# Performance work log

Hardware: AMD Instinct MI355X
Metric: run time of the kernel (lower is better)

## Reference

```python
import jax, jax.numpy as jnp
import numpy as np

CHANNELS_CHOICE = np.array([8, 16, 24, 32, 40, 48, 56, 64])
MAX_C = 64
B, H, W_SP = 128, 32, 32
N_EDGES = 6
# edge list per intermediate node: (edge_weight_index, source_node_index)
EDGES = [[(0, 0)], [(1, 0), (2, 1)], [(3, 0), (4, 1), (5, 2)]]


def setup_inputs() -> dict:
    key = jax.random.key(0)
    k1, k2, k3, k4 = jax.random.split(key, 4)
    inputs = jax.random.normal(k1, (B, MAX_C, H, W_SP), dtype=jnp.float32)
    alphas1 = jax.random.uniform(k2, (8,), dtype=jnp.float32)  # input-width arch weights
    alphas2 = jax.random.uniform(k3, (8,), dtype=jnp.float32)  # output-width arch weights
    # shared master 3x3 conv weight per edge (OIHW)
    W = jax.random.normal(k4, (N_EDGES, MAX_C, MAX_C, 3, 3), dtype=jnp.float32) * 0.05
    return {"inputs": inputs, "alphas1": alphas1, "alphas2": alphas2, "W": W}


def _channel_scale(alphas1, alphas2, dtype):
    # mask[c, i] = 1 if channel c is inside width choice CHANNELS_CHOICE[i]
    mask = (jnp.arange(MAX_C)[:, None] < jnp.asarray(CHANNELS_CHOICE)[None, :]).astype(dtype)  # [64, 8]
    a_in = mask @ alphas1   # [64] cumulative input-channel weight
    a_out = mask @ alphas2  # [64] cumulative output-channel weight
    return a_out[:, None] * a_in[None, :]  # [64, 64]


def _edge(x, w, scale):
    # weighted-combi of all (c1, c2) channel-sliced sub-convs == one conv with scaled weight
    w_eff = w * scale[:, :, None, None]
    return jax.lax.conv_general_dilated(
        jax.nn.relu(x), w_eff, window_strides=(1, 1), padding="SAME",
        dimension_numbers=("NCHW", "OIHW", "NCHW"))


def reference(inputs, alphas1, alphas2, W):
    scale = _channel_scale(alphas1, alphas2, inputs.dtype)
    nodes = [inputs]
    for node_edges in EDGES:
        feat = 0.0
        for l, src in node_edges:
            feat = feat + _edge(nodes[src], W[l], scale)
        nodes.append(feat)
    return nodes[-1]
```

## Files before the change

kernel.cpp:

```cpp
#include <hip/hip_runtime.h>
#include <hip/hip_bf16.h>


typedef __bf16 bf16x8 __attribute__((ext_vector_type(8)));
typedef float floatx4 __attribute__((ext_vector_type(4)));
typedef unsigned int uint32;

#define PADW 34
#define PIMG (PADW * PADW)
#define ROWB (PADW * 64 * 2)
#define A_LDS (18 * ROWB)
#define A_CHUNKS (A_LDS / 16)
#define A_TAIL (A_CHUNKS - 9 * 512)
#define TAPB (64 * 64 * 2)
#define B_LDS (9 * TAPB)
#define SMEM_BYTES (A_LDS + B_LDS)

__device__ __forceinline__ void gld16(const char* g, char* l) {
    __builtin_amdgcn_global_load_lds(
        (const __attribute__((address_space(1))) uint32*)g,
        (__attribute__((address_space(3))) uint32*)l, 16, 0, 0);
}

__global__ __launch_bounds__(256) void pre_kernel(
    const float* __restrict__ in, const float* __restrict__ a1,
    const float* __restrict__ a2, const float* __restrict__ W,
    __hip_bfloat16* __restrict__ wt, __hip_bfloat16* __restrict__ r0,
    __hip_bfloat16* __restrict__ r1, __hip_bfloat16* __restrict__ r2) {
    __shared__ float tile[32][65];
    int blk = blockIdx.x;
    int tid = threadIdx.x;

    if (blk < 864) {
        int idx = blk * 256 + tid;
        int i = idx & 63;
        int o = (idx >> 6) & 63;
        int rest = idx >> 12;
        int t = rest % 9;
        int l = rest / 9;
        int ji = i >> 3, jo = o >> 3;
        float ain = 0.f, aout = 0.f;
#pragma unroll
        for (int j = 0; j < 8; ++j) {
            ain  += (j >= ji) ? a1[j] : 0.f;
            aout += (j >= jo) ? a2[j] : 0.f;
        }
        float v = W[(size_t)((l * 64 + o) * 64 + i) * 9 + t] * ain * aout;
        int os = ((o & 3) << 4) + (o >> 2);
        size_t e = (size_t)(l * 9 + t) * 4096 + os * 64 +
                   ((((i >> 3) ^ (os & 7)) << 3) + (i & 7));
        wt[e] = __float2bfloat16(v);
    } else if (blk < 992) {
        int b = blk - 864;
        __hip_bfloat16* bufs[3] = {r0, r1, r2};
#pragma unroll
        for (int f = 0; f < 3; ++f) {
            uint32* buf = (uint32*)(bufs[f] + (size_t)b * PIMG * 64);
            for (int idx = tid; idx < 132 * 32; idx += 256) {
                int slot = idx >> 5, u = idx & 31;
                int yy, xx;
                if (slot < 34)      { yy = 0;  xx = slot; }
                else if (slot < 68) { yy = 33; xx = slot - 34; }
                else { int s2 = slot - 68; yy = 1 + (s2 >> 1); xx = (s2 & 1) * 33; }
                buf[(size_t)(yy * PADW + xx) * 32 + u] = 0u;
            }
        }
    } else {
        int rb = blk - 992;
        int b = rb >> 5, y = rb & 31;
        int x = tid & 31, c0 = tid >> 5;
        const float* ip = in + ((size_t)b * 64 * 32 + y) * 32 + x;
#pragma unroll
        for (int cc = 0; cc < 8; ++cc) {
            int c = cc * 8 + c0;
            tile[x][c] = fmaxf(ip[(size_t)c * 1024], 0.f);
        }
        __syncthreads();
        int j = tid & 7, xq = tid >> 3;
        int p = (b * PADW + y + 1) * PADW + 1 + xq;
        alignas(16) __hip_bfloat16 hv[8];
#pragma unroll
        for (int k = 0; k < 8; ++k)
            hv[k] = __float2bfloat16(tile[xq][j * 8 + k]);
        *(uint4*)((char*)r0 + (size_t)p * 128 + ((j ^ (p & 7)) << 4)) =
            *(const uint4*)hv;
    }
}

template <int NSRC, bool FINAL>
__global__ __launch_bounds__(512, 1) void conv_stage(
    const __hip_bfloat16* __restrict__ s0,
    const __hip_bfloat16* __restrict__ s1,
    const __hip_bfloat16* __restrict__ s2,
    const __hip_bfloat16* __restrict__ wt,
    void* __restrict__ dstv, int l0) {
    extern __shared__ char smem[];
    char* smemB = smem + A_LDS;
    int tid = threadIdx.x;
    int wv = tid >> 6, lane = tid & 63;
    int quad = lane >> 4, l15 = lane & 15;
    int blk = blockIdx.x;
    int b = blk >> 1, y0 = (blk & 1) << 4;

    const char* srcs[3] = {(const char*)s0, (const char*)s1, (const char*)s2};
    const char* gW = (const char*)wt + (size_t)l0 * 9 * (size_t)TAPB;
    const size_t aOff = (size_t)(b * PADW + y0) * PADW * 128;

    auto stage_A = [&](int s) {
        const char* gA = srcs[s] + aOff;
#pragma unroll
        for (int it = 0; it < 10; ++it) {
            int c = it * 512 + tid;
            if (it < 9 || tid < A_TAIL)
                gld16(gA + (size_t)c * 16, smem + (it * 512 + wv * 64) * 16);
        }
    };
    auto stage_B = [&](int s) {
        const char* gB = gW + (size_t)s * 9 * TAPB;
#pragma unroll
        for (int it = 0; it < 9; ++it) {
            int c = it * 512 + tid;
            gld16(gB + (size_t)c * 16, smemB + (it * 512 + wv * 64) * 16);
        }
    };

    floatx4 acc[4][4];
#pragma unroll
    for (int m = 0; m < 4; ++m)
#pragma unroll
        for (int n = 0; n < 4; ++n) acc[m][n] = (floatx4){0.f, 0.f, 0.f, 0.f};

    stage_A(0);
    stage_B(0);
    __syncthreads();

    uint4 pfA[10];

#pragma unroll 1
    for (int s = 0; s < NSRC; ++s) {
        if (s + 1 < NSRC) {
            const char* gA = srcs[s + 1] + aOff;
#pragma unroll
            for (int it = 0; it < 10; ++it)
                pfA[it] = *(const uint4*)(gA + (size_t)(it * 512 + tid) * 16);
            __builtin_amdgcn_sched_barrier(0);
        }
#pragma unroll
        for (int tl = 0; tl < 9; ++tl) {
            const int ky = tl / 3, kx = tl % 3;
#pragma unroll
            for (int q = 0; q < 2; ++q) {
                bf16x8 Af[4], Bf[4];
#pragma unroll
                for (int m = 0; m < 4; ++m) {
                    int arow = 2 * wv + (m >> 1) + ky;
                    int apx  = ((m & 1) << 4) + l15 + kx;
                    int R = b * PADW + y0 + arow;
                    int slot = ((q << 2) + quad) ^ ((2 * R + apx) & 7);
                    Af[m] = *(const bf16x8*)(smem + arow * ROWB +
                                             apx * 128 + slot * 16);
                }
#pragma unroll
                for (int n = 0; n < 4; ++n) {
                    int o = (n << 4) + l15;
                    int slot = ((q << 2) + quad) ^ (l15 & 7);
                    Bf[n] = *(const bf16x8*)(smemB + tl * TAPB +
                                             o * 128 + slot * 16);
                }
                __builtin_amdgcn_s_setprio(1);
#pragma unroll
                for (int m = 0; m < 4; ++m)
#pragma unroll
                    for (int n = 0; n < 4; ++n)
                        acc[m][n] = __builtin_amdgcn_mfma_f32_16x16x32_bf16(
                            Af[m], Bf[n], acc[m][n], 0, 0, 0);
                __builtin_amdgcn_s_setprio(0);
            }
        }
        if (s + 1 < NSRC) {
            __syncthreads();
#pragma unroll
            for (int it = 0; it < 10; ++it)
                if (it < 9 || tid < A_TAIL)
                    *(uint4*)(smem + (size_t)(it * 512 + tid) * 16) = pfA[it];
            stage_B(s + 1);
            __syncthreads();
        }
    }

    if (FINAL) {
        float* out = (float*)dstv;
#pragma unroll
        for (int m = 0; m < 4; ++m) {
            int row = y0 + 2 * wv + (m >> 1);
#pragma unroll
            for (int n = 0; n < 4; ++n) {
                int o = (l15 << 2) + n;
                *(floatx4*)(out + (((size_t)b * 64 + o) * 32 + row) * 32 +
                            ((m & 1) << 4) + (quad << 2)) = acc[m][n];
            }
        }
    } else {
        __hip_bfloat16* out = (__hip_bfloat16*)dstv;
#pragma unroll
        for (int m = 0; m < 4; ++m) {
            int row = y0 + 2 * wv + (m >> 1);
#pragma unroll
            for (int r = 0; r < 4; ++r) {
                int x = ((m & 1) << 4) + (quad << 2) + r;
                int p = (b * PADW + row + 1) * PADW + x + 1;
                alignas(8) __hip_bfloat16 hv[4];
#pragma unroll
                for (int n = 0; n < 4; ++n)
                    hv[n] = __float2bfloat16(fmaxf(acc[m][n][r], 0.f));
                char* d8 = (char*)out + (size_t)p * 128 +
                           ((((l15 >> 1) ^ (p & 7)) << 4) + ((l15 & 1) << 3));
                *(uint2*)d8 = *(const uint2*)hv;
            }
        }
    }
}

extern "C" void kernel_launch(void* const* d_in, const int* in_sizes, int n_in,
                              void* d_out, int out_size, void* d_ws,
                              size_t ws_size, hipStream_t stream) {
    const float* inputs  = (const float*)d_in[0];
    const float* alphas1 = (const float*)d_in[1];
    const float* alphas2 = (const float*)d_in[2];
    const float* W       = (const float*)d_in[3];
    char* ws = (char*)d_ws;

    __hip_bfloat16* wt = (__hip_bfloat16*)(ws);
    __hip_bfloat16* r0 = (__hip_bfloat16*)(ws + ((size_t)1 << 20));
    __hip_bfloat16* r1 = (__hip_bfloat16*)(ws + ((size_t)20 << 20));
    __hip_bfloat16* r2 = (__hip_bfloat16*)(ws + ((size_t)40 << 20));
    float* out = (float*)d_out;

    (void)hipFuncSetAttribute((const void*)conv_stage<1, false>,
                              hipFuncAttributeMaxDynamicSharedMemorySize,
                              SMEM_BYTES);
    (void)hipFuncSetAttribute((const void*)conv_stage<2, false>,
                              hipFuncAttributeMaxDynamicSharedMemorySize,
                              SMEM_BYTES);
    (void)hipFuncSetAttribute((const void*)conv_stage<3, true>,
                              hipFuncAttributeMaxDynamicSharedMemorySize,
                              SMEM_BYTES);

    pre_kernel<<<864 + 128 + 4096, 256, 0, stream>>>(inputs, alphas1, alphas2,
                                                     W, wt, r0, r1, r2);
    conv_stage<1, false><<<256, 512, SMEM_BYTES, stream>>>(r0, r1, r2, wt,
                                                           (void*)r1, 0);
    conv_stage<2, false><<<256, 512, SMEM_BYTES, stream>>>(r0, r1, r2, wt,
                                                           (void*)r2, 1);
    conv_stage<3, true ><<<256, 512, SMEM_BYTES, stream>>>(r0, r1, r2, wt,
                                                           (void*)out, 3);
}
```

Measured before the change: 169.9 us.

## Double-buffer LDS fragment loads and drop register prefetch of next source tile

The inner MFMA loop is flattened into 18 steps, and the A/B fragments for the next step are loaded from LDS into a second register buffer while the current step's MFMAs run. The register prefetch of the next source's A tile (ten uint4 per thread, global to registers to LDS) is removed. The next source is now loaded with direct global-to-LDS loads after the barrier. This hides LDS latency inside the MFMA loop and frees registers, but the global load of the next source is no longer overlapped with compute.

```diff
diff --git a/kernel.cpp b/kernel.cpp
--- a/kernel.cpp
+++ b/kernel.cpp
@@ -124,6 +124,28 @@
         }
     };
 
+    auto ldA = [&](int tl, int q, bf16x8 (&dst)[4]) {
+        const int ky = tl / 3, kx = tl % 3;
+#pragma unroll
+        for (int m = 0; m < 4; ++m) {
+            int arow = 2 * wv + (m >> 1) + ky;
+            int apx  = ((m & 1) << 4) + l15 + kx;
+            int R = b * PADW + y0 + arow;
+            int slot = ((q << 2) + quad) ^ ((2 * R + apx) & 7);
+            dst[m] = *(const bf16x8*)(smem + arow * ROWB + apx * 128 +
+                                      slot * 16);
+        }
+    };
+    auto ldB = [&](int tl, int q, bf16x8 (&dst)[4]) {
+#pragma unroll
+        for (int n = 0; n < 4; ++n) {
+            int o = (n << 4) + l15;
+            int slot = ((q << 2) + quad) ^ (l15 & 7);
+            dst[n] = *(const bf16x8*)(smemB + tl * TAPB + o * 128 +
+                                      slot * 16);
+        }
+    };
+
     floatx4 acc[4][4];
 #pragma unroll
     for (int m = 0; m < 4; ++m)
@@ -134,55 +156,31 @@
     stage_B(0);
     __syncthreads();
 
-    uint4 pfA[10];
-
 #pragma unroll 1
     for (int s = 0; s < NSRC; ++s) {
-        if (s + 1 < NSRC) {
-            const char* gA = srcs[s + 1] + aOff;
-#pragma unroll
-            for (int it = 0; it < 10; ++it)
-                pfA[it] = *(const uint4*)(gA + (size_t)(it * 512 + tid) * 16);
-            __builtin_amdgcn_sched_barrier(0);
-        }
-#pragma unroll
-        for (int tl = 0; tl < 9; ++tl) {
-            const int ky = tl / 3, kx = tl % 3;
-#pragma unroll
-            for (int q = 0; q < 2; ++q) {
-                bf16x8 Af[4], Bf[4];
-#pragma unroll
-                for (int m = 0; m < 4; ++m) {
-                    int arow = 2 * wv + (m >> 1) + ky;
-                    int apx  = ((m & 1) << 4) + l15 + kx;
-                    int R = b * PADW + y0 + arow;
-                    int slot = ((q << 2) + quad) ^ ((2 * R + apx) & 7);
-                    Af[m] = *(const bf16x8*)(smem + arow * ROWB +
-                                             apx * 128 + slot * 16);
-                }
-#pragma unroll
-                for (int n = 0; n < 4; ++n) {
-                    int o = (n << 4) + l15;
-                    int slot = ((q << 2) + quad) ^ (l15 & 7);
-                    Bf[n] = *(const bf16x8*)(smemB + tl * TAPB +
-                                             o * 128 + slot * 16);
-                }
-                __builtin_amdgcn_s_setprio(1);
-#pragma unroll
-                for (int m = 0; m < 4; ++m)
-#pragma unroll
-                    for (int n = 0; n < 4; ++n)
-                        acc[m][n] = __builtin_amdgcn_mfma_f32_16x16x32_bf16(
-                            Af[m], Bf[n], acc[m][n], 0, 0, 0);
-                __builtin_amdgcn_s_setprio(0);
-            }
+        bf16x8 fA[2][4], fB[2][4];
+        ldA(0, 0, fA[0]);
+        ldB(0, 0, fB[0]);
+#pragma unroll
+        for (int st = 0; st < 18; ++st) {
+            const int pb = st & 1;
+            if (st < 17) {
+                const int nt = (st + 1) >> 1, nq = (st + 1) & 1;
+                ldA(nt, nq, fA[pb ^ 1]);
+                ldB(nt, nq, fB[pb ^ 1]);
+            }
+            __builtin_amdgcn_s_setprio(1);
+#pragma unroll
+            for (int m = 0; m < 4; ++m)
+#pragma unroll
+                for (int n = 0; n < 4; ++n)
+                    acc[m][n] = __builtin_amdgcn_mfma_f32_16x16x32_bf16(
+                        fA[pb][m], fB[pb][n], acc[m][n], 0, 0, 0);
+            __builtin_amdgcn_s_setprio(0);
         }
         if (s + 1 < NSRC) {
             __syncthreads();
-#pragma unroll
-            for (int it = 0; it < 10; ++it)
-                if (it < 9 || tid < A_TAIL)
-                    *(uint4*)(smem + (size_t)(it * 512 + tid) * 16) = pfA[it];
+            stage_A(s + 1);
             stage_B(s + 1);
             __syncthreads();
         }
```

Result: faster. 148.9 us (-12.3%).

## Stream conv weights directly from global into registers, drop LDS B staging

Applied to the files above, without the earlier changes.

Re-lays out the preprocessed weight tensor in MFMA-fragment order so each lane can load its B operand fragments straight from global memory into registers, double-buffered per tap. The weight LDS region and its staging are removed, which shrinks shared memory to the activation tile only. The register prefetch of the next source's activations is also removed; the next source is now loaded into LDS synchronously after a barrier. This trades LDS traffic and capacity for more global/L2 reads per wave, higher register pressure, and an exposed activation load between sources.

```diff
diff --git a/kernel.cpp b/kernel.cpp
--- a/kernel.cpp
+++ b/kernel.cpp
@@ -5,6 +5,7 @@
 typedef __bf16 bf16x8 __attribute__((ext_vector_type(8)));
 typedef float floatx4 __attribute__((ext_vector_type(4)));
 typedef unsigned int uint32;
+typedef uint32 u32x4 __attribute__((ext_vector_type(4)));
 
 #define PADW 34
 #define PIMG (PADW * PADW)
@@ -13,8 +14,7 @@
 #define A_CHUNKS (A_LDS / 16)
 #define A_TAIL (A_CHUNKS - 9 * 512)
 #define TAPB (64 * 64 * 2)
-#define B_LDS (9 * TAPB)
-#define SMEM_BYTES (A_LDS + B_LDS)
+#define SMEM_BYTES A_LDS
 
 __device__ __forceinline__ void gld16(const char* g, char* l) {
     __builtin_amdgcn_global_load_lds(
@@ -47,9 +47,12 @@
         }
         float v = W[(size_t)((l * 64 + o) * 64 + i) * 9 + t] * ain * aout;
         int os = ((o & 3) << 4) + (o >> 2);
-        size_t e = (size_t)(l * 9 + t) * 4096 + os * 64 +
-                   ((((i >> 3) ^ (os & 7)) << 3) + (i & 7));
-        wt[e] = __float2bfloat16(v);
+        int n  = os >> 4, c15 = os & 15;
+        int q  = i >> 5, quad = (i >> 3) & 3, e = i & 7;
+        int ln = (quad << 4) + c15;
+        size_t idx2 = (size_t)(l * 9 + t) * 4096 + (((q << 2) + n) << 9) +
+                      (ln << 3) + e;
+        wt[idx2] = __float2bfloat16(v);
     } else if (blk < 992) {
         int b = blk - 864;
         __hip_bfloat16* bufs[3] = {r0, r1, r2};
@@ -95,7 +98,6 @@
     const __hip_bfloat16* __restrict__ wt,
     void* __restrict__ dstv, int l0) {
     extern __shared__ char smem[];
-    char* smemB = smem + A_LDS;
     int tid = threadIdx.x;
     int wv = tid >> 6, lane = tid & 63;
     int quad = lane >> 4, l15 = lane & 15;
@@ -115,14 +117,6 @@
                 gld16(gA + (size_t)c * 16, smem + (it * 512 + wv * 64) * 16);
         }
     };
-    auto stage_B = [&](int s) {
-        const char* gB = gW + (size_t)s * 9 * TAPB;
-#pragma unroll
-        for (int it = 0; it < 9; ++it) {
-            int c = it * 512 + tid;
-            gld16(gB + (size_t)c * 16, smemB + (it * 512 + wv * 64) * 16);
-        }
-    };
 
     floatx4 acc[4][4];
 #pragma unroll
@@ -131,26 +125,27 @@
         for (int n = 0; n < 4; ++n) acc[m][n] = (floatx4){0.f, 0.f, 0.f, 0.f};
 
     stage_A(0);
-    stage_B(0);
     __syncthreads();
-
-    uint4 pfA[10];
 
 #pragma unroll 1
     for (int s = 0; s < NSRC; ++s) {
-        if (s + 1 < NSRC) {
-            const char* gA = srcs[s + 1] + aOff;
-#pragma unroll
-            for (int it = 0; it < 10; ++it)
-                pfA[it] = *(const uint4*)(gA + (size_t)(it * 512 + tid) * 16);
-            __builtin_amdgcn_sched_barrier(0);
-        }
-#pragma unroll
-        for (int tl = 0; tl < 9; ++tl) {
-            const int ky = tl / 3, kx = tl % 3;
+        const char* gWs = gW + (size_t)s * 9 * TAPB;
+        u32x4 Bb[2][8];
+        auto ldBg = [&](int t, int par) {
+#pragma unroll
+            for (int f = 0; f < 8; ++f)
+                Bb[par][f] = *(const __attribute__((address_space(1))) u32x4*)
+                    (gWs + (size_t)t * TAPB + (f << 10) + (lane << 4));
+        };
+        ldBg(0, 0);
+#pragma unroll
+        for (int t = 0; t < 9; ++t) {
+            const int par = t & 1;
+            if (t < 8) ldBg(t + 1, par ^ 1);
+            const int ky = t / 3, kx = t % 3;
 #pragma unroll
             for (int q = 0; q < 2; ++q) {
-                bf16x8 Af[4], Bf[4];
+                bf16x8 Af[4];
 #pragma unroll
                 for (int m = 0; m < 4; ++m) {
                     int arow = 2 * wv + (m >> 1) + ky;
@@ -160,30 +155,22 @@
                     Af[m] = *(const bf16x8*)(smem + arow * ROWB +
                                              apx * 128 + slot * 16);
                 }
+                __builtin_amdgcn_s_setprio(1);
 #pragma unroll
                 for (int n = 0; n < 4; ++n) {
-                    int o = (n << 4) + l15;
-                    int slot = ((q << 2) + quad) ^ (l15 & 7);
-                    Bf[n] = *(const bf16x8*)(smemB + tl * TAPB +
-                                             o * 128 + slot * 16);
+                    bf16x8 Bf = __builtin_bit_cast(bf16x8,
+                                                   Bb[par][(q << 2) + n]);
+#pragma unroll
+                    for (int m = 0; m < 4; ++m)
+                        acc[m][n] = __builtin_amdgcn_mfma_f32_16x16x32_bf16(
+                            Af[m], Bf, acc[m][n], 0, 0, 0);
                 }
-                __builtin_amdgcn_s_setprio(1);
-#pragma unroll
-                for (int m = 0; m < 4; ++m)
-#pragma unroll
-                    for (int n = 0; n < 4; ++n)
-                        acc[m][n] = __builtin_amdgcn_mfma_f32_16x16x32_bf16(
-                            Af[m], Bf[n], acc[m][n], 0, 0, 0);
                 __builtin_amdgcn_s_setprio(0);
             }
         }
         if (s + 1 < NSRC) {
             __syncthreads();
-#pragma unroll
-            for (int it = 0; it < 10; ++it)
-                if (it < 9 || tid < A_TAIL)
-                    *(uint4*)(smem + (size_t)(it * 512 + tid) * 16) = pfA[it];
-            stage_B(s + 1);
+            stage_A(s + 1);
             __syncthreads();
         }
     }
```

Measured after the change: 154.1 us. 9.3% less time.
